# Kernel optimization log

Hardware: AMD Instinct MI355X
Metric: run time of the kernel (lower is better)

## Reference

```python
import jax, jax.numpy as jnp
import numpy as np

N_RES = 3      # n_resblock (weights SHARED across layers, matching [block]*n in torch)
N_E = 1024     # n_embeddings
E_DIM = 64     # dim_embeddings
P = 4
BETA = 0.25
B = 16384      # batch rows
IN = 128       # input_size
DENC = 512     # dim_encoder
DOUT = E_DIM * P  # dim_encoder_out = 256


def setup_inputs() -> dict:
    key = jax.random.key(0)
    ks = jax.random.split(key, 16)
    def w(k, o, i):
        return jax.random.normal(k, (o, i), jnp.float32) * 0.02
    return {
        "x": jax.random.normal(ks[0], (B, IN), jnp.float32),
        "a": jax.random.normal(ks[1], (B, IN), jnp.float32),
        "scale": 1.0 + 0.1 * jax.random.normal(ks[2], (IN,), jnp.float32),
        "shift": 0.01 * jax.random.normal(ks[3], (IN,), jnp.float32),
        "enc_win_w": w(ks[4], DENC, IN), "enc_win_b": jnp.zeros((DENC,), jnp.float32),
        "enc_ain_w": w(ks[5], DENC, IN), "enc_ain_b": jnp.zeros((DENC,), jnp.float32),
        "enc_wres_w": w(ks[6], DENC, DENC), "enc_wres_b": jnp.zeros((DENC,), jnp.float32),
        "enc_wres_g": jnp.ones((DENC,), jnp.float32), "enc_wres_be": jnp.zeros((DENC,), jnp.float32),
        "enc_ares_w": w(ks[7], DENC, DENC), "enc_ares_b": jnp.zeros((DENC,), jnp.float32),
        "enc_ares_g": jnp.ones((DENC,), jnp.float32), "enc_ares_be": jnp.zeros((DENC,), jnp.float32),
        "enc_out_w": w(ks[8], DOUT, DENC), "enc_out_b": jnp.zeros((DOUT,), jnp.float32),
        "dec1_w": w(ks[9], DENC, DOUT), "dec1_b": jnp.zeros((DENC,), jnp.float32),
        "dec_res_w": w(ks[10], DENC, DENC), "dec_res_b": jnp.zeros((DENC,), jnp.float32),
        "dec_res_g": jnp.ones((DENC,), jnp.float32), "dec_res_be": jnp.zeros((DENC,), jnp.float32),
        "dec2_w": w(ks[11], IN, DENC), "dec2_b": jnp.zeros((IN,), jnp.float32),
        "codebook": jax.random.uniform(ks[12], (N_E, E_DIM), jnp.float32, -1.0 / N_E, 1.0 / N_E),
    }


def _ln(h, g, b, eps=1e-5):
    m = jnp.mean(h, axis=-1, keepdims=True)
    v = jnp.var(h, axis=-1, keepdims=True)
    return (h - m) * jax.lax.rsqrt(v + eps) * g + b


def _resblock(x, w, b, g, be):
    # Linear -> LayerNorm -> ReLU, residual add
    h = x @ w.T + b
    return x + jax.nn.relu(_ln(h, g, be))


def reference(x, a, scale, shift,
              enc_win_w, enc_win_b, enc_ain_w, enc_ain_b,
              enc_wres_w, enc_wres_b, enc_wres_g, enc_wres_be,
              enc_ares_w, enc_ares_b, enc_ares_g, enc_ares_be,
              enc_out_w, enc_out_b,
              dec1_w, dec1_b,
              dec_res_w, dec_res_b, dec_res_g, dec_res_be,
              dec2_w, dec2_b, codebook):
    sg = jax.lax.stop_gradient
    # --- input normalization ---
    xs = (x - shift) / scale
    # --- Encoder (weight path modulated by activation-magnitude path) ---
    av = a @ enc_ain_w.T + enc_ain_b
    h = xs @ enc_win_w.T + enc_win_b
    for _ in range(N_RES):  # shared weights per stack, interleaved mul
        av = _resblock(av, enc_ares_w, enc_ares_b, enc_ares_g, enc_ares_be)
        h = _resblock(h, enc_wres_w, enc_wres_b, enc_wres_g, enc_wres_be) * av
    z_e = h @ enc_out_w.T + enc_out_b  # (B, P*E_DIM)
    # --- Vector quantization (cdist + argmin + gather) ---
    zf = z_e.reshape(-1, E_DIM)  # (B*P, E_DIM)
    d = (jnp.sum(zf * zf, axis=1, keepdims=True)
         + jnp.sum(codebook * codebook, axis=1)
         - 2.0 * zf @ codebook.T)  # (B*P, N_E)
    idx = jnp.argmin(d, axis=1)  # (B*P,)
    z_q = codebook[idx].reshape(z_e.shape)
    loss = (jnp.mean((sg(z_q) - z_e) ** 2)
            + BETA * jnp.mean((z_q - sg(z_e)) ** 2))
    z_q_st = z_e + sg(z_q - z_e)  # straight-through
    counts = jnp.zeros((N_E,), jnp.float32).at[idx].add(1.0)
    e_mean = counts / zf.shape[0]
    perplexity = jnp.exp(-jnp.sum(e_mean * jnp.log(e_mean + 1e-10)))
    # --- Decoder ---
    hd = z_q_st @ dec1_w.T + dec1_b
    for _ in range(N_RES):
        hd = _resblock(hd, dec_res_w, dec_res_b, dec_res_g, dec_res_be)
    x_hat = hd @ dec2_w.T + dec2_b
    x_hat = scale * x_hat + shift
    return (loss, x_hat, perplexity, z_q_st, idx)
```

## Files before the change

kernel.cpp:

```cpp
#include <hip/hip_runtime.h>
#include <hip/hip_bf16.h>
#include <math.h>

static constexpr int BROWS = 16384;
static constexpr int IND   = 128;
static constexpr int DE    = 512;
static constexpr int DOUTD = 256;
static constexpr int ED    = 64;
static constexpr int NE    = 1024;

static constexpr size_t O_XHAT = 1;
static constexpr size_t O_PERP = 2097153;
static constexpr size_t O_ZQ   = 2097154;
static constexpr size_t O_IDX  = 6291458;

typedef __attribute__((ext_vector_type(8))) short short8v;
typedef __attribute__((ext_vector_type(4))) float f32x4;
typedef __attribute__((ext_vector_type(4))) unsigned short ushort4v;
typedef __attribute__((ext_vector_type(8))) unsigned short ushort8v;

__device__ inline float wave_sum(float v) {
#pragma unroll
    for (int o = 32; o >= 1; o >>= 1) v += __shfl_xor(v, o, 64);
    return v;
}

__device__ inline unsigned short f2bf(float f) {
    unsigned u = __float_as_uint(f);
    return (unsigned short)((u + 0x7FFFu + ((u >> 16) & 1u)) >> 16);
}
__device__ inline float bf2f(unsigned short b) {
    return __uint_as_float(((unsigned)b) << 16);
}
struct Split3 { unsigned short b0, b1, b2; };
__device__ inline Split3 split3(float v) {
    Split3 s;
    s.b0 = f2bf(v);  float r  = v - bf2f(s.b0);
    s.b1 = f2bf(r);  float r2 = r - bf2f(s.b1);
    s.b2 = f2bf(r2);
    return s;
}

template<int K, int EPI>
__device__ inline void gemm8_body(const unsigned short* __restrict__ A0, const unsigned short* __restrict__ A1,
                                  const unsigned short* __restrict__ A2,
                                  const unsigned short* __restrict__ W0, const unsigned short* __restrict__ W1,
                                  const unsigned short* __restrict__ W2,
                                  const float* __restrict__ bias, float* __restrict__ Cf,
                                  unsigned short* __restrict__ S0, unsigned short* __restrict__ S1,
                                  unsigned short* __restrict__ S2, int N,
                                  short (*As)[128 * 40], short (*Ws)[128 * 40])
{
    const int t = threadIdx.x;
    const int bm = blockIdx.x << 7, bn = blockIdx.y << 7;
    const int lane = t & 63, wid = t >> 6;
    const int wm = (wid >> 1) << 6, wn = (wid & 1) << 6;
    const int lr = lane & 15, lg = lane >> 4;
    const unsigned short* Ap[3] = {A0, A1, A2};
    const unsigned short* Wp[3] = {W0, W1, W2};
    f32x4 acc[4][4] = {};
    for (int k0 = 0; k0 < K; k0 += 32) {
#pragma unroll
        for (int p = 0; p < 3; ++p) {
#pragma unroll
            for (int s = 0; s < 2; ++s) {
                int c = t + (s << 8);
                int row = c >> 2, kc = (c & 3) << 3;
                *(short8v*)&As[p][row * 40 + kc] =
                    *(const short8v*)(Ap[p] + (size_t)(bm + row) * K + k0 + kc);
                *(short8v*)&Ws[p][row * 40 + kc] =
                    *(const short8v*)(Wp[p] + (size_t)(bn + row) * K + k0 + kc);
            }
        }
        __syncthreads();
        short8v bfr[3][4];
#pragma unroll
        for (int p = 0; p < 3; ++p)
#pragma unroll
            for (int nj = 0; nj < 4; ++nj)
                bfr[p][nj] = *(const short8v*)&Ws[p][(wn + nj * 16 + lr) * 40 + lg * 8];
#pragma unroll
        for (int mi = 0; mi < 4; ++mi) {
            short8v a0 = *(const short8v*)&As[0][(wm + mi * 16 + lr) * 40 + lg * 8];
            short8v a1 = *(const short8v*)&As[1][(wm + mi * 16 + lr) * 40 + lg * 8];
            short8v a2 = *(const short8v*)&As[2][(wm + mi * 16 + lr) * 40 + lg * 8];
#pragma unroll
            for (int nj = 0; nj < 4; ++nj) {
                f32x4 c = acc[mi][nj];
                c = __builtin_amdgcn_mfma_f32_16x16x32_bf16(a2, bfr[1][nj], c, 0, 0, 0);
                c = __builtin_amdgcn_mfma_f32_16x16x32_bf16(a1, bfr[2][nj], c, 0, 0, 0);
                c = __builtin_amdgcn_mfma_f32_16x16x32_bf16(a1, bfr[1][nj], c, 0, 0, 0);
                c = __builtin_amdgcn_mfma_f32_16x16x32_bf16(a2, bfr[0][nj], c, 0, 0, 0);
                c = __builtin_amdgcn_mfma_f32_16x16x32_bf16(a0, bfr[2][nj], c, 0, 0, 0);
                c = __builtin_amdgcn_mfma_f32_16x16x32_bf16(a1, bfr[0][nj], c, 0, 0, 0);
                c = __builtin_amdgcn_mfma_f32_16x16x32_bf16(a0, bfr[1][nj], c, 0, 0, 0);
                c = __builtin_amdgcn_mfma_f32_16x16x32_bf16(a0, bfr[0][nj], c, 0, 0, 0);
                acc[mi][nj] = c;
            }
        }
        __syncthreads();
    }
#pragma unroll
    for (int mi = 0; mi < 4; ++mi)
#pragma unroll
        for (int nj = 0; nj < 4; ++nj)
#pragma unroll
            for (int r = 0; r < 4; ++r) {
                int m = bm + wm + mi * 16 + lg * 4 + r;
                int n = bn + wn + nj * 16 + lr;
                float v = acc[mi][nj][r] + bias[n];
                if (EPI == 0) {
                    Cf[(size_t)m * N + n] = v;
                } else {
                    Split3 sp = split3(v);
                    S0[(size_t)m * N + n] = sp.b0;
                    S1[(size_t)m * N + n] = sp.b1;
                    S2[(size_t)m * N + n] = sp.b2;
                }
            }
}

template<int K>
__global__ __launch_bounds__(256)
void gemm8_k(const unsigned short* __restrict__ A0, const unsigned short* __restrict__ A1,
             const unsigned short* __restrict__ A2,
             const unsigned short* __restrict__ W0, const unsigned short* __restrict__ W1,
             const unsigned short* __restrict__ W2,
             const float* __restrict__ bias, float* __restrict__ C, int N)
{
    __shared__ short As[3][128 * 40];
    __shared__ short Ws[3][128 * 40];
    gemm8_body<K, 0>(A0, A1, A2, W0, W1, W2, bias, C, nullptr, nullptr, nullptr, N, As, Ws);
}

struct G8 { const unsigned short *A0, *A1, *A2, *W0, *W1, *W2; const float* bias;
            float* Cf; unsigned short *S0, *S1, *S2; };

template<int K, int EPI>
__global__ __launch_bounds__(256)
void gemm8pair_k(G8 ga, G8 gb, int N)
{
    __shared__ short As[3][128 * 40];
    __shared__ short Ws[3][128 * 40];
    const G8& g = (blockIdx.z == 0) ? ga : gb;
    gemm8_body<K, EPI>(g.A0, g.A1, g.A2, g.W0, g.W1, g.W2, g.bias, g.Cf,
                       g.S0, g.S1, g.S2, N, As, Ws);
}

template<int K, int EPI>
__global__ __launch_bounds__(256)
void gemmbf_k(const short* __restrict__ A, const short* __restrict__ W,
              const float* __restrict__ bias, float* __restrict__ C, int N,
              unsigned short* __restrict__ Cb,
              const float* __restrict__ escale, const float* __restrict__ eshift)
{
    __shared__ short As[128 * 40];
    __shared__ short Ws[128 * 40];
    const int t = threadIdx.x;
    const int bm = blockIdx.x << 7, bn = blockIdx.y << 7;
    const int lane = t & 63, wid = t >> 6;
    const int wm = (wid >> 1) << 6, wn = (wid & 1) << 6;
    const int lr = lane & 15, lg = lane >> 4;
    f32x4 acc[4][4] = {};
    for (int k0 = 0; k0 < K; k0 += 32) {
#pragma unroll
        for (int s = 0; s < 2; ++s) {
            int c = t + (s << 8);
            int row = c >> 2, kc = (c & 3) << 3;
            *(short8v*)&As[row * 40 + kc] = *(const short8v*)(A + (size_t)(bm + row) * K + k0 + kc);
            *(short8v*)&Ws[row * 40 + kc] = *(const short8v*)(W + (size_t)(bn + row) * K + k0 + kc);
        }
        __syncthreads();
        short8v af[4], bf[4];
#pragma unroll
        for (int mi = 0; mi < 4; ++mi) af[mi] = *(const short8v*)&As[(wm + mi * 16 + lr) * 40 + lg * 8];
#pragma unroll
        for (int nj = 0; nj < 4; ++nj) bf[nj] = *(const short8v*)&Ws[(wn + nj * 16 + lr) * 40 + lg * 8];
#pragma unroll
        for (int mi = 0; mi < 4; ++mi)
#pragma unroll
            for (int nj = 0; nj < 4; ++nj)
                acc[mi][nj] = __builtin_amdgcn_mfma_f32_16x16x32_bf16(af[mi], bf[nj], acc[mi][nj], 0, 0, 0);
        __syncthreads();
    }
#pragma unroll
    for (int mi = 0; mi < 4; ++mi)
#pragma unroll
        for (int nj = 0; nj < 4; ++nj)
#pragma unroll
            for (int r = 0; r < 4; ++r) {
                int m = bm + wm + mi * 16 + lg * 4 + r;
                int n = bn + wn + nj * 16 + lr;
                float v = acc[mi][nj][r] + bias[n];
                if (EPI == 2) v = escale[n] * v + eshift[n];
                C[(size_t)m * N + n] = v;
                if (EPI == 1) Cb[(size_t)m * N + n] = f2bf(v);
            }
}

__global__ __launch_bounds__(256)
void prep2_k(const float* __restrict__ x, const float* __restrict__ scale,
             const float* __restrict__ shift,
             unsigned short* __restrict__ x0, unsigned short* __restrict__ x1,
             unsigned short* __restrict__ x2,
             const float* __restrict__ a,
             unsigned short* __restrict__ a0, unsigned short* __restrict__ a1,
             unsigned short* __restrict__ a2)
{
    if (blockIdx.x < 2048) {
        int g = blockIdx.x * 256 + threadIdx.x;
        float4 v = *(const float4*)(x + (size_t)g * 4);
        int col = (g * 4) & (IND - 1);
        float vals[4] = {v.x, v.y, v.z, v.w};
        ushort4v o0, o1, o2;
#pragma unroll
        for (int i = 0; i < 4; ++i) {
            float xs = (vals[i] - shift[col + i]) / scale[col + i];
            Split3 s = split3(xs);
            o0[i] = s.b0; o1[i] = s.b1; o2[i] = s.b2;
        }
        *(ushort4v*)(x0 + (size_t)g * 4) = o0;
        *(ushort4v*)(x1 + (size_t)g * 4) = o1;
        *(ushort4v*)(x2 + (size_t)g * 4) = o2;
    } else {
        int g = (blockIdx.x - 2048) * 256 + threadIdx.x;
        float4 v = *(const float4*)(a + (size_t)g * 4);
        float vals[4] = {v.x, v.y, v.z, v.w};
        ushort4v o0, o1, o2;
#pragma unroll
        for (int i = 0; i < 4; ++i) {
            Split3 s = split3(vals[i]);
            o0[i] = s.b0; o1[i] = s.b1; o2[i] = s.b2;
        }
        *(ushort4v*)(a0 + (size_t)g * 4) = o0;
        *(ushort4v*)(a1 + (size_t)g * 4) = o1;
        *(ushort4v*)(a2 + (size_t)g * 4) = o2;
    }
}

__global__ __launch_bounds__(256)
void wsplit_k(const float* __restrict__ ain_w, const float* __restrict__ win_w,
              const float* __restrict__ ares_w, const float* __restrict__ wres_w,
              const float* __restrict__ out_w,
              unsigned short* __restrict__ wsb)
{
    int g4 = blockIdx.x * 256 + threadIdx.x;
    const float* src; unsigned short *d0, *d1, *d2; int base;
    if (g4 < 16384)       { src = ain_w;  d0 = wsb;           d1 = wsb + 65536;   d2 = wsb + 131072;  base = 0; }
    else if (g4 < 32768)  { src = win_w;  d0 = wsb + 196608;  d1 = wsb + 262144;  d2 = wsb + 327680;  base = 16384; }
    else if (g4 < 98304)  { src = ares_w; d0 = wsb + 393216;  d1 = wsb + 655360;  d2 = wsb + 917504;  base = 32768; }
    else if (g4 < 163840) { src = wres_w; d0 = wsb + 1179648; d1 = wsb + 1441792; d2 = wsb + 1703936; base = 98304; }
    else                  { src = out_w;  d0 = wsb + 1966080; d1 = wsb + 2097152; d2 = wsb + 2228224; base = 163840; }
    int l4 = g4 - base;
    float4 v = *(const float4*)(src + (size_t)l4 * 4);
    float vals[4] = {v.x, v.y, v.z, v.w};
    ushort4v o0, o1, o2;
#pragma unroll
    for (int i = 0; i < 4; ++i) {
        Split3 s = split3(vals[i]);
        o0[i] = s.b0; o1[i] = s.b1; o2[i] = s.b2;
    }
    *(ushort4v*)(d0 + (size_t)l4 * 4) = o0;
    *(ushort4v*)(d1 + (size_t)l4 * 4) = o1;
    *(ushort4v*)(d2 + (size_t)l4 * 4) = o2;
}

__global__ __launch_bounds__(256)
void cvt3_k(const float* __restrict__ dec1_w, const float* __restrict__ dres_w,
            const float* __restrict__ dec2_w,
            unsigned short* __restrict__ w1b, unsigned short* __restrict__ wrb,
            unsigned short* __restrict__ w2b)
{
    int g = blockIdx.x * 256 + threadIdx.x;
    if (g < 131072)       w1b[g] = f2bf(dec1_w[g]);
    else if (g < 393216)  wrb[g - 131072] = f2bf(dres_w[g - 131072]);
    else if (g < 458752)  w2b[g - 393216] = f2bf(dec2_w[g - 393216]);
}

__global__ __launch_bounds__(256)
void ln_enc2s_k(const float* __restrict__ T1, const float* __restrict__ T2,
                unsigned short* __restrict__ a0, unsigned short* __restrict__ a1,
                unsigned short* __restrict__ a2,
                unsigned short* __restrict__ h0, unsigned short* __restrict__ h1,
                unsigned short* __restrict__ h2,
                const float* __restrict__ ag, const float* __restrict__ abe,
                const float* __restrict__ wg, const float* __restrict__ wbe)
{
    const int lane = threadIdx.x & 63;
    const int row  = (blockIdx.x << 2) + (threadIdx.x >> 6);
    const int col  = lane << 3;
    const size_t base = (size_t)row * DE + col;
    float t[8];
    { float4 p0 = *(const float4*)(T1 + base); float4 p1 = *(const float4*)(T1 + base + 4);
      t[0]=p0.x; t[1]=p0.y; t[2]=p0.z; t[3]=p0.w; t[4]=p1.x; t[5]=p1.y; t[6]=p1.z; t[7]=p1.w; }
    float s = 0.f;
#pragma unroll
    for (int i = 0; i < 8; ++i) s += t[i];
    s = wave_sum(s);
    float mean = s * (1.0f / 512.0f);
    float vs = 0.f;
#pragma unroll
    for (int i = 0; i < 8; ++i) { float d = t[i] - mean; vs += d * d; }
    vs = wave_sum(vs);
    float rstd = 1.0f / sqrtf(vs * (1.0f / 512.0f) + 1e-5f);
    float avn[8];
    {
        ushort8v b0 = *(const ushort8v*)(a0 + base);
        ushort8v b1 = *(const ushort8v*)(a1 + base);
        ushort8v b2 = *(const ushort8v*)(a2 + base);
        ushort8v o0, o1, o2;
#pragma unroll
        for (int i = 0; i < 8; ++i) {
            float avv = bf2f(b0[i]) + bf2f(b1[i]) + bf2f(b2[i]);
            float lnv = (t[i] - mean) * rstd * ag[col + i] + abe[col + i];
            avn[i] = avv + fmaxf(lnv, 0.0f);
            Split3 sp = split3(avn[i]);
            o0[i] = sp.b0; o1[i] = sp.b1; o2[i] = sp.b2;
        }
        *(ushort8v*)(a0 + base) = o0;
        *(ushort8v*)(a1 + base) = o1;
        *(ushort8v*)(a2 + base) = o2;
    }
    { float4 p0 = *(const float4*)(T2 + base); float4 p1 = *(const float4*)(T2 + base + 4);
      t[0]=p0.x; t[1]=p0.y; t[2]=p0.z; t[3]=p0.w; t[4]=p1.x; t[5]=p1.y; t[6]=p1.z; t[7]=p1.w; }
    s = 0.f;
#pragma unroll
    for (int i = 0; i < 8; ++i) s += t[i];
    s = wave_sum(s);
    float mean2 = s * (1.0f / 512.0f);
    vs = 0.f;
#pragma unroll
    for (int i = 0; i < 8; ++i) { float d = t[i] - mean2; vs += d * d; }
    vs = wave_sum(vs);
    float rstd2 = 1.0f / sqrtf(vs * (1.0f / 512.0f) + 1e-5f);
    {
        ushort8v b0 = *(const ushort8v*)(h0 + base);
        ushort8v b1 = *(const ushort8v*)(h1 + base);
        ushort8v b2 = *(const ushort8v*)(h2 + base);
        ushort8v o0, o1, o2;
#pragma unroll
        for (int i = 0; i < 8; ++i) {
            float hv  = bf2f(b0[i]) + bf2f(b1[i]) + bf2f(b2[i]);
            float lnv = (t[i] - mean2) * rstd2 * wg[col + i] + wbe[col + i];
            float hn  = (hv + fmaxf(lnv, 0.0f)) * avn[i];
            Split3 sp = split3(hn);
            o0[i] = sp.b0; o1[i] = sp.b1; o2[i] = sp.b2;
        }
        *(ushort8v*)(h0 + base) = o0;
        *(ushort8v*)(h1 + base) = o1;
        *(ushort8v*)(h2 + base) = o2;
    }
}

__global__ __launch_bounds__(256)
void ln_dec_k(const float* __restrict__ t_, float* __restrict__ h,
              const float* __restrict__ g, const float* __restrict__ be,
              unsigned short* __restrict__ hb)
{
    const int lane = threadIdx.x & 63;
    const int row  = (blockIdx.x << 2) + (threadIdx.x >> 6);
    const int col  = lane << 3;
    const size_t base = (size_t)row * DE + col;
    float t[8];
    { float4 p0 = *(const float4*)(t_ + base); float4 p1 = *(const float4*)(t_ + base + 4);
      t[0]=p0.x; t[1]=p0.y; t[2]=p0.z; t[3]=p0.w; t[4]=p1.x; t[5]=p1.y; t[6]=p1.z; t[7]=p1.w; }
    float s = 0.f;
#pragma unroll
    for (int i = 0; i < 8; ++i) s += t[i];
    s = wave_sum(s);
    float mean = s * (1.0f / 512.0f);
    float vs = 0.f;
#pragma unroll
    for (int i = 0; i < 8; ++i) { float d = t[i] - mean; vs += d * d; }
    vs = wave_sum(vs);
    float rstd = 1.0f / sqrtf(vs * (1.0f / 512.0f) + 1e-5f);
    float4 p0 = *(const float4*)(h + base); float4 p1 = *(const float4*)(h + base + 4);
    float hv[8] = {p0.x,p0.y,p0.z,p0.w,p1.x,p1.y,p1.z,p1.w};
    float hn[8];
    ushort8v ob;
#pragma unroll
    for (int i = 0; i < 8; ++i) {
        float lnv = (t[i] - mean) * rstd * g[col + i] + be[col + i];
        hn[i] = hv[i] + fmaxf(lnv, 0.0f);
        ob[i] = f2bf(hn[i]);
    }
    float4 o0 = {hn[0],hn[1],hn[2],hn[3]}, o1 = {hn[4],hn[5],hn[6],hn[7]};
    *(float4*)(h + base) = o0; *(float4*)(h + base + 4) = o1;
    *(ushort8v*)(hb + base) = ob;
}

__global__ __launch_bounds__(256)
void c2z_k(const float* __restrict__ cb, float* __restrict__ c2, int* __restrict__ counts)
{
    int j = blockIdx.x * 256 + threadIdx.x;
    if (j < NE) {
        float s = 0.f;
        const float* p = cb + (size_t)j * ED;
#pragma unroll
        for (int d = 0; d < ED; ++d) s = fmaf(p[d], p[d], s);
        c2[j] = s;
        counts[j] = 0;
    }
}

__global__ __launch_bounds__(256)
void vq_k(const float* __restrict__ ze, const float* __restrict__ cb, const float* __restrict__ c2,
          float* __restrict__ idx_dst, float* __restrict__ zst_dst,
          unsigned short* __restrict__ zb,
          int* __restrict__ counts, float* __restrict__ partials)
{
    __shared__ float zs[64 * 68];
    __shared__ float cbs[64 * 128];
    __shared__ float z2s[64];
    __shared__ float c2s[128];
    __shared__ int   bidxs[64];
    __shared__ float red[4];
    const int t = threadIdx.x;
    const int tx = t & 15, ty = t >> 4;
    const size_t row0 = (size_t)blockIdx.x * 64;

#pragma unroll
    for (int s = 0; s < 4; ++s) {
        int c = t + (s << 8);
        int row = c >> 4, dc = (c & 15) << 2;
        float4 v = *(const float4*)(ze + (row0 + row) * 64 + dc);
        *(float4*)&zs[row * 68 + dc] = v;
    }
    __syncthreads();
    if (t < 64) {
        float z2 = 0.f;
#pragma unroll 8
        for (int d = 0; d < 64; ++d) { float zv = zs[t * 68 + d]; z2 = fmaf(zv, zv, z2); }
        z2s[t] = z2;
    }

    float best[4] = {INFINITY, INFINITY, INFINITY, INFINITY};
    int   bid[4]  = {0, 0, 0, 0};
    for (int t0 = 0; t0 < NE; t0 += 128) {
        __syncthreads();
#pragma unroll
        for (int s = 0; s < 8; ++s) {
            int c = t + (s << 8);
            int code = c >> 4, dc = (c & 15) << 2;
            float4 v = *(const float4*)(cb + (size_t)(t0 + code) * 64 + dc);
            float vv[4] = {v.x, v.y, v.z, v.w};
#pragma unroll
            for (int i = 0; i < 4; ++i) {
                int r = dc + i;
                cbs[r * 128 + (code ^ (((r >> 2) & 7) << 2))] = vv[i];
            }
        }
        if (t < 128) c2s[t] = c2[t0 + t];
        __syncthreads();
        float acc[4][8] = {};
#pragma unroll 4
        for (int kk0 = 0; kk0 < 64; kk0 += 4) {
            float a_[4][4];
#pragma unroll
            for (int r = 0; r < 4; ++r)
                *(float4*)&a_[r][0] = *(const float4*)&zs[(4 * ty + r) * 68 + kk0];
#pragma unroll
            for (int ko = 0; ko < 4; ++ko) {
                int kk = kk0 + ko;
                int sc = ((kk >> 2) & 7) << 2;
                float bv[8];
                *(float4*)&bv[0] = *(const float4*)&cbs[kk * 128 + ((tx << 2) ^ sc)];
                *(float4*)&bv[4] = *(const float4*)&cbs[kk * 128 + 64 + ((tx << 2) ^ sc)];
#pragma unroll
                for (int r = 0; r < 4; ++r)
#pragma unroll
                    for (int j = 0; j < 8; ++j)
                        acc[r][j] = fmaf(a_[r][ko], bv[j], acc[r][j]);
            }
        }
#pragma unroll
        for (int r = 0; r < 4; ++r) {
            float z2v = z2s[(ty << 2) + r];
#pragma unroll
            for (int j = 0; j < 8; ++j) {
                int cloc = (j < 4) ? ((tx << 2) + j) : (64 + (tx << 2) + (j - 4));
                float term = __fadd_rn(z2v, c2s[cloc]);
                float dist = __fsub_rn(term, __fmul_rn(2.0f, acc[r][j]));
                if (dist < best[r]) { best[r] = dist; bid[r] = t0 + cloc; }
            }
        }
    }
    __syncthreads();
    float* rbd = cbs;
    int*   rbi = (int*)(cbs + 1024);
#pragma unroll
    for (int r = 0; r < 4; ++r) {
        rbd[((ty << 2) + r) * 16 + tx] = best[r];
        rbi[((ty << 2) + r) * 16 + tx] = bid[r];
    }
    __syncthreads();
    if (t < 64) {
        float bd = INFINITY; int bi = 0;
#pragma unroll
        for (int q = 0; q < 16; ++q) {
            float d = rbd[t * 16 + q]; int i = rbi[t * 16 + q];
            if (d < bd || (d == bd && i < bi)) { bd = d; bi = i; }
        }
        bidxs[t] = bi;
        idx_dst[row0 + t] = (float)bi;
        atomicAdd(&counts[bi], 1);
    }
    __syncthreads();
    const int row = t >> 2, cq = t & 3;
    const int bi = bidxs[row];
    float lsum = 0.f;
#pragma unroll
    for (int dd = 0; dd < 16; dd += 4) {
        int d0 = (cq << 4) + dd;
        float4 q4 = *(const float4*)(cb + (size_t)bi * 64 + d0);
        float qv[4] = {q4.x, q4.y, q4.z, q4.w};
        float zst[4];
#pragma unroll
        for (int i = 0; i < 4; ++i) {
            float zv = zs[row * 68 + d0 + i];
            float df = qv[i] - zv;
            lsum = fmaf(df, df, lsum);
            zst[i] = __fadd_rn(zv, __fsub_rn(qv[i], zv));
            zb[(row0 + row) * 64 + d0 + i] = f2bf(zst[i]);
        }
        float2 o0 = {zst[0], zst[1]}, o1 = {zst[2], zst[3]};
        *(float2*)(zst_dst + (row0 + row) * 64 + d0) = o0;
        *(float2*)(zst_dst + (row0 + row) * 64 + d0 + 2) = o1;
    }
    lsum = wave_sum(lsum);
    if ((t & 63) == 0) red[t >> 6] = lsum;
    __syncthreads();
    if (t == 0) partials[blockIdx.x] = ((red[0] + red[1]) + red[2]) + red[3];
}

__global__ __launch_bounds__(256)
void fin_k(const float* __restrict__ partials, const int* __restrict__ counts,
           float* __restrict__ loss_out, float* __restrict__ perp_out)
{
    __shared__ float red[4];
    __shared__ float red2[4];
    const int tid = threadIdx.x;
    float v = 0.f;
    for (int c = tid; c < 1024; c += 256) v += partials[c];
    float s = wave_sum(v);
    if ((tid & 63) == 0) red[tid >> 6] = s;
    float ep = 0.f;
    for (int c = tid; c < NE; c += 256) {
        float e = (float)counts[c] * (1.0f / 65536.0f);
        ep += e * logf(e + 1e-10f);
    }
    ep = wave_sum(ep);
    if ((tid & 63) == 0) red2[tid >> 6] = ep;
    __syncthreads();
    if (tid == 0) {
        float S = ((red[0] + red[1]) + red[2]) + red[3];
        float E = ((red2[0] + red2[1]) + red2[2]) + red2[3];
        loss_out[0] = 1.25f * (S * (1.0f / 4194304.0f));
        perp_out[0] = expf(-E);
    }
}

extern "C" void kernel_launch(void* const* d_in, const int* in_sizes, int n_in,
                              void* d_out, int out_size, void* d_ws, size_t ws_size,
                              hipStream_t stream)
{
    const float* x       = (const float*)d_in[0];
    const float* a       = (const float*)d_in[1];
    const float* scale   = (const float*)d_in[2];
    const float* shift   = (const float*)d_in[3];
    const float* win_w   = (const float*)d_in[4];
    const float* win_b   = (const float*)d_in[5];
    const float* ain_w   = (const float*)d_in[6];
    const float* ain_b   = (const float*)d_in[7];
    const float* wres_w  = (const float*)d_in[8];
    const float* wres_b  = (const float*)d_in[9];
    const float* wres_g  = (const float*)d_in[10];
    const float* wres_be = (const float*)d_in[11];
    const float* ares_w  = (const float*)d_in[12];
    const float* ares_b  = (const float*)d_in[13];
    const float* ares_g  = (const float*)d_in[14];
    const float* ares_be = (const float*)d_in[15];
    const float* out_w   = (const float*)d_in[16];
    const float* out_b   = (const float*)d_in[17];
    const float* dec1_w  = (const float*)d_in[18];
    const float* dec1_b  = (const float*)d_in[19];
    const float* dres_w  = (const float*)d_in[20];
    const float* dres_b  = (const float*)d_in[21];
    const float* dres_g  = (const float*)d_in[22];
    const float* dres_be = (const float*)d_in[23];
    const float* dec2_w  = (const float*)d_in[24];
    const float* dec2_b  = (const float*)d_in[25];
    const float* cb      = (const float*)d_in[26];

    float* ws = (float*)d_ws;
    unsigned short* u = (unsigned short*)d_ws;
    unsigned short* avS0 = u;
    unsigned short* avS1 = u + 8388608;
    unsigned short* avS2 = u + 16777216;
    unsigned short* hS0  = u + 25165824;
    unsigned short* hS1  = u + 33554432;
    unsigned short* hS2  = u + 41943040;
    float* T1 = ws + 25165824;
    float* T2 = ws + 29360128;
    float* ZE = ws + 25165824;
    unsigned short* aS0  = u + 50331648, *aS1  = u + 52428800, *aS2  = u + 54525952;
    unsigned short* xsS0 = u + 56623104, *xsS1 = u + 58720256, *xsS2 = u + 60817408;
    unsigned short* ZB  = u;
    unsigned short* w1b = u + 4194304;
    unsigned short* wrb = u + 4325376;
    unsigned short* w2b = u + 4587520;
    float* t_dec = ws + 4194304;
    float* hd    = ws + 12582912;
    unsigned short* Hb = (unsigned short*)(ws + 29360128);
    unsigned short* wsb = u + 67108864;
    unsigned short* ainS0 = wsb,            *ainS1 = wsb + 65536,  *ainS2 = wsb + 131072;
    unsigned short* winS0 = wsb + 196608,   *winS1 = wsb + 262144, *winS2 = wsb + 327680;
    unsigned short* areS0 = wsb + 393216,   *areS1 = wsb + 655360, *areS2 = wsb + 917504;
    unsigned short* wreS0 = wsb + 1179648,  *wreS1 = wsb + 1441792,*wreS2 = wsb + 1703936;
    unsigned short* outS0 = wsb + 1966080,  *outS1 = wsb + 2097152,*outS2 = wsb + 2228224;
    float* c2v      = ws + 34800000;
    int*   counts   = (int*)(ws + 34801024);
    float* partials = ws + 34802048;

    float* dout = (float*)d_out;

    wsplit_k<<<768, 256, 0, stream>>>(ain_w, win_w, ares_w, wres_w, out_w, wsb);
    prep2_k<<<4096, 256, 0, stream>>>(x, scale, shift, xsS0, xsS1, xsS2, a, aS0, aS1, aS2);
    {
        G8 ga = {aS0, aS1, aS2, ainS0, ainS1, ainS2, ain_b, nullptr, avS0, avS1, avS2};
        G8 gb = {xsS0, xsS1, xsS2, winS0, winS1, winS2, win_b, nullptr, hS0, hS1, hS2};
        gemm8pair_k<128, 1><<<dim3(128, 4, 2), 256, 0, stream>>>(ga, gb, DE);
    }
    for (int r = 0; r < 3; ++r) {
        for (int half = 0; half < 2; ++half) {
            const size_t mo = (size_t)half * 8192 * DE;
            G8 ga = {avS0 + mo, avS1 + mo, avS2 + mo, areS0, areS1, areS2, ares_b, T1, nullptr, nullptr, nullptr};
            G8 gb = {hS0 + mo,  hS1 + mo,  hS2 + mo,  wreS0, wreS1, wreS2, wres_b, T2, nullptr, nullptr, nullptr};
            gemm8pair_k<512, 0><<<dim3(64, 4, 2), 256, 0, stream>>>(ga, gb, DE);
            ln_enc2s_k<<<2048, 256, 0, stream>>>(T1, T2,
                avS0 + mo, avS1 + mo, avS2 + mo, hS0 + mo, hS1 + mo, hS2 + mo,
                ares_g, ares_be, wres_g, wres_be);
        }
    }
    gemm8_k<512><<<dim3(128, 2), 256, 0, stream>>>(hS0, hS1, hS2, outS0, outS1, outS2, out_b, ZE, DOUTD);
    c2z_k<<<4, 256, 0, stream>>>(cb, c2v, counts);
    vq_k<<<1024, 256, 0, stream>>>(ZE, cb, c2v, dout + O_IDX, dout + O_ZQ, ZB, counts, partials);
    fin_k<<<1, 256, 0, stream>>>(partials, counts, dout, dout + O_PERP);
    cvt3_k<<<1792, 256, 0, stream>>>(dec1_w, dres_w, dec2_w, w1b, wrb, w2b);
    gemmbf_k<256, 1><<<dim3(128, 4), 256, 0, stream>>>(
        (const short*)ZB, (const short*)w1b, dec1_b, hd, DE, Hb, nullptr, nullptr);
    for (int r = 0; r < 3; ++r) {
        gemmbf_k<512, 0><<<dim3(128, 4), 256, 0, stream>>>(
            (const short*)Hb, (const short*)wrb, dres_b, t_dec, DE, nullptr, nullptr, nullptr);
        ln_dec_k<<<4096, 256, 0, stream>>>(t_dec, hd, dres_g, dres_be, Hb);
    }
    gemmbf_k<512, 2><<<dim3(128, 1), 256, 0, stream>>>(
        (const short*)Hb, (const short*)w2b, dec2_b, dout + O_XHAT, IND, nullptr, scale, shift);
}
```

Measured before the change: 847.9 us.

## Compute VQ distances with split-bf16 MFMA instead of scalar FP32 FMAs

Rewrites the vector-quantization distance kernel so the z·codebook dot products use bf16 MFMA instructions. Both operands are split into three bf16 parts to emulate FP32 precision, and eight cross-product MFMAs are accumulated per k-step. The codebook split is precomputed in the c2 kernel, and the argmin reduction now uses wave shuffles instead of a shared-memory pass. The aim is to cut the scalar FMA cost of the 1024-code distance GEMM. The risk is small rounding differences that could flip near-tie argmin results.

Measured after the change: 817.2 us. 3.6% less time.

```diff
diff --git a/kernel.cpp b/kernel.cpp
--- a/kernel.cpp
+++ b/kernel.cpp
@@ -390,7 +390,9 @@
 }
 
 __global__ __launch_bounds__(256)
-void c2z_k(const float* __restrict__ cb, float* __restrict__ c2, int* __restrict__ counts)
+void c2z_k(const float* __restrict__ cb, float* __restrict__ c2, int* __restrict__ counts,
+           unsigned short* __restrict__ cbS0, unsigned short* __restrict__ cbS1,
+           unsigned short* __restrict__ cbS2)
 {
     int j = blockIdx.x * 256 + threadIdx.x;
     if (j < NE) {
@@ -400,110 +402,144 @@
         for (int d = 0; d < ED; ++d) s = fmaf(p[d], p[d], s);
         c2[j] = s;
         counts[j] = 0;
+#pragma unroll
+        for (int dc = 0; dc < 64; dc += 4) {
+            float4 v = *(const float4*)(p + dc);
+            float vals[4] = {v.x, v.y, v.z, v.w};
+            ushort4v o0, o1, o2;
+#pragma unroll
+            for (int i = 0; i < 4; ++i) {
+                Split3 sp = split3(vals[i]);
+                o0[i] = sp.b0; o1[i] = sp.b1; o2[i] = sp.b2;
+            }
+            *(ushort4v*)(cbS0 + (size_t)j * 64 + dc) = o0;
+            *(ushort4v*)(cbS1 + (size_t)j * 64 + dc) = o1;
+            *(ushort4v*)(cbS2 + (size_t)j * 64 + dc) = o2;
+        }
     }
 }
 
 __global__ __launch_bounds__(256)
 void vq_k(const float* __restrict__ ze, const float* __restrict__ cb, const float* __restrict__ c2,
+          const unsigned short* __restrict__ cbS0, const unsigned short* __restrict__ cbS1,
+          const unsigned short* __restrict__ cbS2,
           float* __restrict__ idx_dst, float* __restrict__ zst_dst,
           unsigned short* __restrict__ zb,
           int* __restrict__ counts, float* __restrict__ partials)
 {
-    __shared__ float zs[64 * 68];
-    __shared__ float cbs[64 * 128];
+    __shared__ unsigned short zA[3][64 * 64];
+    __shared__ unsigned short cB[3][64 * 64];
     __shared__ float z2s[64];
-    __shared__ float c2s[128];
+    __shared__ float c2s[64];
     __shared__ int   bidxs[64];
     __shared__ float red[4];
     const int t = threadIdx.x;
-    const int tx = t & 15, ty = t >> 4;
+    const int lane = t & 63, w = t >> 6;
     const size_t row0 = (size_t)blockIdx.x * 64;
 
 #pragma unroll
-    for (int s = 0; s < 4; ++s) {
+    for (int s = 0; s < 2; ++s) {
         int c = t + (s << 8);
-        int row = c >> 4, dc = (c & 15) << 2;
-        float4 v = *(const float4*)(ze + (row0 + row) * 64 + dc);
-        *(float4*)&zs[row * 68 + dc] = v;
-    }
-    __syncthreads();
+        int row = c >> 3, kb = c & 7;
+        float4 v0 = *(const float4*)(ze + (row0 + row) * 64 + kb * 8);
+        float4 v1 = *(const float4*)(ze + (row0 + row) * 64 + kb * 8 + 4);
+        float vals[8] = {v0.x, v0.y, v0.z, v0.w, v1.x, v1.y, v1.z, v1.w};
+        ushort8v o0, o1, o2;
+#pragma unroll
+        for (int i = 0; i < 8; ++i) {
+            Split3 sp = split3(vals[i]);
+            o0[i] = sp.b0; o1[i] = sp.b1; o2[i] = sp.b2;
+        }
+        int base = row * 64 + ((kb ^ (row & 7)) << 3);
+        *(ushort8v*)&zA[0][base] = o0;
+        *(ushort8v*)&zA[1][base] = o1;
+        *(ushort8v*)&zA[2][base] = o2;
+    }
     if (t < 64) {
         float z2 = 0.f;
+        const float* zp = ze + (row0 + t) * 64;
 #pragma unroll 8
-        for (int d = 0; d < 64; ++d) { float zv = zs[t * 68 + d]; z2 = fmaf(zv, zv, z2); }
+        for (int d = 0; d < 64; ++d) z2 = fmaf(zp[d], zp[d], z2);
         z2s[t] = z2;
+    }
+    __syncthreads();
+
+    short8v af[2][3];
+    {
+        int row = (w << 4) + (lane & 15);
+#pragma unroll
+        for (int ks = 0; ks < 2; ++ks) {
+            int kb = (lane >> 4) + ks * 4;
+            int base = row * 64 + ((kb ^ (row & 7)) << 3);
+#pragma unroll
+            for (int p = 0; p < 3; ++p)
+                af[ks][p] = *(const short8v*)&zA[p][base];
+        }
     }
 
     float best[4] = {INFINITY, INFINITY, INFINITY, INFINITY};
     int   bid[4]  = {0, 0, 0, 0};
-    for (int t0 = 0; t0 < NE; t0 += 128) {
+    for (int t0 = 0; t0 < NE; t0 += 64) {
         __syncthreads();
 #pragma unroll
-        for (int s = 0; s < 8; ++s) {
+        for (int s = 0; s < 2; ++s) {
             int c = t + (s << 8);
-            int code = c >> 4, dc = (c & 15) << 2;
-            float4 v = *(const float4*)(cb + (size_t)(t0 + code) * 64 + dc);
-            float vv[4] = {v.x, v.y, v.z, v.w};
-#pragma unroll
-            for (int i = 0; i < 4; ++i) {
-                int r = dc + i;
-                cbs[r * 128 + (code ^ (((r >> 2) & 7) << 2))] = vv[i];
+            int code = c >> 3, kb = c & 7;
+            int gbase = (t0 + code) * 64 + kb * 8;
+            int lbase = code * 64 + ((kb ^ (code & 7)) << 3);
+            *(ushort8v*)&cB[0][lbase] = *(const ushort8v*)(cbS0 + gbase);
+            *(ushort8v*)&cB[1][lbase] = *(const ushort8v*)(cbS1 + gbase);
+            *(ushort8v*)&cB[2][lbase] = *(const ushort8v*)(cbS2 + gbase);
+        }
+        if (t < 64) c2s[t] = c2[t0 + t];
+        __syncthreads();
+
+#pragma unroll
+        for (int ct = 0; ct < 4; ++ct) {
+            f32x4 acc = {0.f, 0.f, 0.f, 0.f};
+            int code = (ct << 4) + (lane & 15);
+#pragma unroll
+            for (int ks = 0; ks < 2; ++ks) {
+                int kb = (lane >> 4) + ks * 4;
+                int base = code * 64 + ((kb ^ (code & 7)) << 3);
+                short8v b0 = *(const short8v*)&cB[0][base];
+                short8v b1 = *(const short8v*)&cB[1][base];
+                short8v b2 = *(const short8v*)&cB[2][base];
+                acc = __builtin_amdgcn_mfma_f32_16x16x32_bf16(af[ks][2], b1, acc, 0, 0, 0);
+                acc = __builtin_amdgcn_mfma_f32_16x16x32_bf16(af[ks][1], b2, acc, 0, 0, 0);
+                acc = __builtin_amdgcn_mfma_f32_16x16x32_bf16(af[ks][1], b1, acc, 0, 0, 0);
+                acc = __builtin_amdgcn_mfma_f32_16x16x32_bf16(af[ks][2], b0, acc, 0, 0, 0);
+                acc = __builtin_amdgcn_mfma_f32_16x16x32_bf16(af[ks][0], b2, acc, 0, 0, 0);
+                acc = __builtin_amdgcn_mfma_f32_16x16x32_bf16(af[ks][1], b0, acc, 0, 0, 0);
+                acc = __builtin_amdgcn_mfma_f32_16x16x32_bf16(af[ks][0], b1, acc, 0, 0, 0);
+                acc = __builtin_amdgcn_mfma_f32_16x16x32_bf16(af[ks][0], b0, acc, 0, 0, 0);
             }
-        }
-        if (t < 128) c2s[t] = c2[t0 + t];
-        __syncthreads();
-        float acc[4][8] = {};
-#pragma unroll 4
-        for (int kk0 = 0; kk0 < 64; kk0 += 4) {
-            float a_[4][4];
-#pragma unroll
-            for (int r = 0; r < 4; ++r)
-                *(float4*)&a_[r][0] = *(const float4*)&zs[(4 * ty + r) * 68 + kk0];
-#pragma unroll
-            for (int ko = 0; ko < 4; ++ko) {
-                int kk = kk0 + ko;
-                int sc = ((kk >> 2) & 7) << 2;
-                float bv[8];
-                *(float4*)&bv[0] = *(const float4*)&cbs[kk * 128 + ((tx << 2) ^ sc)];
-                *(float4*)&bv[4] = *(const float4*)&cbs[kk * 128 + 64 + ((tx << 2) ^ sc)];
-#pragma unroll
-                for (int r = 0; r < 4; ++r)
-#pragma unroll
-                    for (int j = 0; j < 8; ++j)
-                        acc[r][j] = fmaf(a_[r][ko], bv[j], acc[r][j]);
+            float c2v = c2s[(ct << 4) + (lane & 15)];
+            int gcode = t0 + (ct << 4) + (lane & 15);
+#pragma unroll
+            for (int r = 0; r < 4; ++r) {
+                float z2v = z2s[(w << 4) + ((lane >> 4) << 2) + r];
+                float term = __fadd_rn(z2v, c2v);
+                float dist = __fsub_rn(term, __fmul_rn(2.0f, acc[r]));
+                if (dist < best[r]) { best[r] = dist; bid[r] = gcode; }
             }
         }
-#pragma unroll
-        for (int r = 0; r < 4; ++r) {
-            float z2v = z2s[(ty << 2) + r];
-#pragma unroll
-            for (int j = 0; j < 8; ++j) {
-                int cloc = (j < 4) ? ((tx << 2) + j) : (64 + (tx << 2) + (j - 4));
-                float term = __fadd_rn(z2v, c2s[cloc]);
-                float dist = __fsub_rn(term, __fmul_rn(2.0f, acc[r][j]));
-                if (dist < best[r]) { best[r] = dist; bid[r] = t0 + cloc; }
-            }
-        }
-    }
-    __syncthreads();
-    float* rbd = cbs;
-    int*   rbi = (int*)(cbs + 1024);
+    }
 #pragma unroll
     for (int r = 0; r < 4; ++r) {
-        rbd[((ty << 2) + r) * 16 + tx] = best[r];
-        rbi[((ty << 2) + r) * 16 + tx] = bid[r];
-    }
-    __syncthreads();
-    if (t < 64) {
-        float bd = INFINITY; int bi = 0;
-#pragma unroll
-        for (int q = 0; q < 16; ++q) {
-            float d = rbd[t * 16 + q]; int i = rbi[t * 16 + q];
-            if (d < bd || (d == bd && i < bi)) { bd = d; bi = i; }
-        }
-        bidxs[t] = bi;
-        idx_dst[row0 + t] = (float)bi;
-        atomicAdd(&counts[bi], 1);
+        float bd = best[r]; int bi = bid[r];
+#pragma unroll
+        for (int m = 1; m < 16; m <<= 1) {
+            float od = __shfl_xor(bd, m, 64);
+            int   oi = __shfl_xor(bi, m, 64);
+            if (od < bd || (od == bd && oi < bi)) { bd = od; bi = oi; }
+        }
+        if ((lane & 15) == 0) {
+            int row = (w << 4) + ((lane >> 4) << 2) + r;
+            bidxs[row] = bi;
+            idx_dst[row0 + row] = (float)bi;
+            atomicAdd(&counts[bi], 1);
+        }
     }
     __syncthreads();
     const int row = t >> 2, cq = t & 3;
@@ -514,10 +550,12 @@
         int d0 = (cq << 4) + dd;
         float4 q4 = *(const float4*)(cb + (size_t)bi * 64 + d0);
         float qv[4] = {q4.x, q4.y, q4.z, q4.w};
+        float4 zv4 = *(const float4*)(ze + (row0 + row) * 64 + d0);
+        float zvv[4] = {zv4.x, zv4.y, zv4.z, zv4.w};
         float zst[4];
 #pragma unroll
         for (int i = 0; i < 4; ++i) {
-            float zv = zs[row * 68 + d0 + i];
+            float zv = zvv[i];
             float df = qv[i] - zv;
             lsum = fmaf(df, df, lsum);
             zst[i] = __fadd_rn(zv, __fsub_rn(qv[i], zv));
@@ -621,6 +659,9 @@
     float* c2v      = ws + 34800000;
     int*   counts   = (int*)(ws + 34801024);
     float* partials = ws + 34802048;
+    unsigned short* cbS0 = u + 69606144;
+    unsigned short* cbS1 = u + 69671680;
+    unsigned short* cbS2 = u + 69737216;
 
     float* dout = (float*)d_out;
 
@@ -643,8 +684,9 @@
         }
     }
     gemm8_k<512><<<dim3(128, 2), 256, 0, stream>>>(hS0, hS1, hS2, outS0, outS1, outS2, out_b, ZE, DOUTD);
-    c2z_k<<<4, 256, 0, stream>>>(cb, c2v, counts);
-    vq_k<<<1024, 256, 0, stream>>>(ZE, cb, c2v, dout + O_IDX, dout + O_ZQ, ZB, counts, partials);
+    c2z_k<<<4, 256, 0, stream>>>(cb, c2v, counts, cbS0, cbS1, cbS2);
+    vq_k<<<1024, 256, 0, stream>>>(ZE, cb, c2v, cbS0, cbS1, cbS2,
+                                   dout + O_IDX, dout + O_ZQ, ZB, counts, partials);
     fin_k<<<1, 256, 0, stream>>>(partials, counts, dout, dout + O_PERP);
     cvt3_k<<<1792, 256, 0, stream>>>(dec1_w, dres_w, dec2_w, w1b, wrb, w2b);
     gemmbf_k<256, 1><<<dim3(128, 4), 256, 0, stream>>>(
```
